# Kernel tuning notes

Measured on AMD Instinct MI355X. Metric: run time of the kernel, lower is better.

Reference implementation:

```python
import jax, jax.numpy as jnp
import numpy as np
import math

B, H, S, D = 2, 16, 2048, 64

def setup_inputs() -> dict:
    key = jax.random.key(0)
    kq, kk, kv = jax.random.split(key, 3)
    Q = jax.random.normal(kq, (B, H, S, D), dtype=jnp.float32)
    K = jax.random.normal(kk, (B, H, S, D), dtype=jnp.float32)
    V = jax.random.normal(kv, (B, H, S, D), dtype=jnp.float32)
    causal_mask = jnp.tril(jnp.ones((S, S), dtype=bool))
    return {"Q": Q, "K": K, "V": V, "causal_mask": causal_mask}

def reference(Q, K, V, causal_mask):
    d_k = K.shape[-1]
    scores = jnp.einsum('bhqd,bhkd->bhqk', Q, K) / math.sqrt(d_k)
    scores = jnp.where(causal_mask, scores, -jnp.inf)
    probs = jax.nn.softmax(scores, axis=-1)
    return jnp.einsum('bhqk,bhkd->bhqd', probs, V)
```

## Files before the change

kernel.cpp:

```cpp
#include <hip/hip_runtime.h>
#include <math.h>


constexpr int kS   = 2048;
constexpr int kD   = 64;
constexpr int kBH  = 32;
constexpr int kPadP = 72;
constexpr int kFragBH = 64 * 4 * 512;

typedef short short8 __attribute__((ext_vector_type(8)));
typedef float float4v __attribute__((ext_vector_type(4)));
typedef float float16v __attribute__((ext_vector_type(16)));
typedef unsigned int u32;
typedef unsigned short u16;

static __device__ inline u16 f2bf(float f) {
  union { float f; unsigned u; } v; v.f = f;
  unsigned r = v.u + 0x7FFF + ((v.u >> 16) & 1);
  return (u16)(r >> 16);
}

static __device__ inline short8 pack8(float4v a, float4v b) {
  short8 r;
  r[0] = (short)f2bf(a[0]); r[1] = (short)f2bf(a[1]);
  r[2] = (short)f2bf(a[2]); r[3] = (short)f2bf(a[3]);
  r[4] = (short)f2bf(b[0]); r[5] = (short)f2bf(b[1]);
  r[6] = (short)f2bf(b[2]); r[7] = (short)f2bf(b[3]);
  return r;
}

static __device__ inline void swap32(u32 a, u32 b, u32& oa, u32& ob) {
#if __has_builtin(__builtin_amdgcn_permlane32_swap)
  auto r = __builtin_amdgcn_permlane32_swap(a, b, false, false);
  oa = r[0]; ob = r[1];
#else
  asm volatile("v_permlane32_swap_b32 %0, %1" : "+v"(a), "+v"(b));
  oa = a; ob = b;
#endif
}

__global__ __launch_bounds__(256)
void prep_kernel(const float* __restrict__ Q, const float* __restrict__ K,
                 const float* __restrict__ V,
                 u16* __restrict__ Qf, u16* __restrict__ Kf, u16* __restrict__ Vf) {
  __shared__ u16 tile[64 * kPadP];
  const int tid = threadIdx.x;
  const int bh = blockIdx.y, st = blockIdx.x;
  const size_t ibase = (size_t)bh * kS * kD + (size_t)st * 64 * kD;
  const size_t fbase = (size_t)bh * kFragBH;
  const int r  = tid >> 2;
  const int c0 = (tid & 3) * 16;
  const int dk = tid & 3;
  const int U  = st * 2 + (r >> 5);
  const int lr = r & 31;
  {
    const float scl = 0.125f * 1.44269504089f;
    const float* qp = Q + ibase + (size_t)r * kD + c0;
    float4v a = *(const float4v*)(qp);
    float4v b = *(const float4v*)(qp + 4);
    float4v c = *(const float4v*)(qp + 8);
    float4v d = *(const float4v*)(qp + 12);
    #pragma unroll
    for (int i = 0; i < 4; ++i) { a[i] *= scl; b[i] *= scl; c[i] *= scl; d[i] *= scl; }
    u16* dst = Qf + fbase + (size_t)(U * 4 + dk) * 512;
    *(short8*)(dst + lr * 8)        = pack8(a, b);
    *(short8*)(dst + (32 + lr) * 8) = pack8(c, d);
  }
  {
    const float* kp = K + ibase + (size_t)r * kD + c0;
    float4v a = *(const float4v*)(kp);
    float4v b = *(const float4v*)(kp + 4);
    float4v c = *(const float4v*)(kp + 8);
    float4v d = *(const float4v*)(kp + 12);
    u16* dst = Kf + fbase + (size_t)(U * 4 + dk) * 512;
    *(short8*)(dst + lr * 8)        = pack8(a, b);
    *(short8*)(dst + (32 + lr) * 8) = pack8(c, d);
  }
  {
    const float* vp = V + ibase + (size_t)r * kD + c0;
    float4v a = *(const float4v*)(vp);
    float4v b = *(const float4v*)(vp + 4);
    float4v c = *(const float4v*)(vp + 8);
    float4v d = *(const float4v*)(vp + 12);
    u16* t = &tile[r * kPadP + c0];
    *(short8*)t       = pack8(a, b);
    *(short8*)(t + 8) = pack8(c, d);
  }
  __syncthreads();
  {
    const int dd = tid >> 2;
    const int s0 = (tid & 3) * 16;
    short8 w0, w1;
    #pragma unroll
    for (int i = 0; i < 8; ++i) {
      w0[i] = (short)tile[(s0 + i) * kPadP + dd];
      w1[i] = (short)tile[(s0 + 8 + i) * kPadP + dd];
    }
    const int ku   = st * 2 + (s0 >> 5);
    const int koff = s0 & 31;
    const int c    = ((koff >> 4) << 1) | (dd >> 5);
    u16* vdst = Vf + fbase + (size_t)(ku * 4 + c) * 512;
    *(short8*)(vdst + (dd & 31) * 8)        = w0;
    *(short8*)(vdst + (32 + (dd & 31)) * 8) = w1;
  }
}

__global__ __launch_bounds__(64, 2)
void fattn_kernel(const u16* __restrict__ Qf, const u16* __restrict__ Kf,
                  const u16* __restrict__ Vf, float* __restrict__ O) {
  const int lane = threadIdx.x;
  const int l31  = lane & 31;
  const int h    = lane >> 5;

  const int orig = ((blockIdx.x & 7) << 8) | (blockIdx.x >> 3);
  const int pr   = orig >> 7;
  const int r2   = orig & 127;
  const int s    = 63 - (r2 >> 1);
  const int bh   = pr * 2 + (r2 & 1);
  const int q0   = s * 32;

  const size_t fb = (size_t)bh * kFragBH;
  const u16* kp = Kf + fb + lane * 8;
  const u16* vp = Vf + fb + lane * 8;

  float16v zf;
  #pragma unroll
  for (int i = 0; i < 16; ++i) zf[i] = 0.f;

  short8 ones;
  #pragma unroll
  for (int i = 0; i < 8; ++i) ones[i] = (short)0x3F80;

  short8 qf[4];
  {
    const u16* qp = Qf + fb + (size_t)(s * 4) * 512 + lane * 8;
    #pragma unroll
    for (int dk = 0; dk < 4; ++dk) qf[dk] = *(const short8*)(qp + dk * 512);
  }

  float16v acc0 = zf, acc1 = zf, lacc = zf;
  const int qg = q0 + l31;

  short8 kA[4], vA[4], kB[4], vB[4];
  #pragma unroll
  for (int dk = 0; dk < 4; ++dk) kA[dk] = *(const short8*)(kp + dk * 512);
  #pragma unroll
  for (int c = 0; c < 4; ++c)    vA[c]  = *(const short8*)(vp + c * 512);

  auto step = [&](const short8* kc, const short8* vc, short8* kn, short8* vn, int k) {
    const int knext = (k < s) ? (k + 1) : k;
    #pragma unroll
    for (int dk = 0; dk < 4; ++dk) kn[dk] = *(const short8*)(kp + knext * 2048 + dk * 512);
    #pragma unroll
    for (int c = 0; c < 4; ++c)    vn[c]  = *(const short8*)(vp + knext * 2048 + c * 512);

    __builtin_amdgcn_s_setprio(1);
    float16v sv = __builtin_amdgcn_mfma_f32_32x32x16_bf16(kc[0], qf[0], zf, 0, 0, 0);
    sv = __builtin_amdgcn_mfma_f32_32x32x16_bf16(kc[1], qf[1], sv, 0, 0, 0);
    sv = __builtin_amdgcn_mfma_f32_32x32x16_bf16(kc[2], qf[2], sv, 0, 0, 0);
    sv = __builtin_amdgcn_mfma_f32_32x32x16_bf16(kc[3], qf[3], sv, 0, 0, 0);
    __builtin_amdgcn_s_setprio(0);

    if (k == s) {
      #pragma unroll
      for (int r = 0; r < 16; ++r) {
        const int kg = k * 32 + (r & 3) + 8 * (r >> 2) + 4 * h;
        if (kg > qg) sv[r] = -1e30f;
      }
    }

    u32 pk[8];
    #pragma unroll
    for (int g2 = 0; g2 < 4; ++g2) {
      const u32 u0 = __float_as_uint(__builtin_amdgcn_exp2f(sv[4 * g2 + 0]));
      const u32 u1 = __float_as_uint(__builtin_amdgcn_exp2f(sv[4 * g2 + 1]));
      const u32 u2 = __float_as_uint(__builtin_amdgcn_exp2f(sv[4 * g2 + 2]));
      const u32 u3 = __float_as_uint(__builtin_amdgcn_exp2f(sv[4 * g2 + 3]));
      pk[2 * g2]     = __builtin_amdgcn_perm(u1, u0, 0x07060302u);
      pk[2 * g2 + 1] = __builtin_amdgcn_perm(u3, u2, 0x07060302u);
    }

    {
      union { u32 u[4]; short8 s8; } pf;
      swap32(pk[0], pk[2], pf.u[0], pf.u[2]);
      swap32(pk[1], pk[3], pf.u[1], pf.u[3]);
      __builtin_amdgcn_s_setprio(1);
      acc0 = __builtin_amdgcn_mfma_f32_32x32x16_bf16(pf.s8, vc[0], acc0, 0, 0, 0);
      acc1 = __builtin_amdgcn_mfma_f32_32x32x16_bf16(pf.s8, vc[1], acc1, 0, 0, 0);
      lacc = __builtin_amdgcn_mfma_f32_32x32x16_bf16(pf.s8, ones,  lacc, 0, 0, 0);
      __builtin_amdgcn_s_setprio(0);
    }
    {
      union { u32 u[4]; short8 s8; } pf;
      swap32(pk[4], pk[6], pf.u[0], pf.u[2]);
      swap32(pk[5], pk[7], pf.u[1], pf.u[3]);
      __builtin_amdgcn_s_setprio(1);
      acc0 = __builtin_amdgcn_mfma_f32_32x32x16_bf16(pf.s8, vc[2], acc0, 0, 0, 0);
      acc1 = __builtin_amdgcn_mfma_f32_32x32x16_bf16(pf.s8, vc[3], acc1, 0, 0, 0);
      lacc = __builtin_amdgcn_mfma_f32_32x32x16_bf16(pf.s8, ones,  lacc, 0, 0, 0);
      __builtin_amdgcn_s_setprio(0);
    }
  };

  int k = 0;
  while (true) {
    step(kA, vA, kB, vB, k); if (++k > s) break;
    step(kB, vB, kA, vA, k); if (++k > s) break;
  }

  #pragma unroll
  for (int r = 0; r < 16; ++r) {
    const int row = (r & 3) + 8 * (r >> 2) + 4 * h;
    const float inv = 1.f / lacc[r];
    float* op = O + ((size_t)bh * kS + q0 + row) * kD;
    op[l31]      = acc0[r] * inv;
    op[l31 + 32] = acc1[r] * inv;
  }
}

extern "C" void kernel_launch(void* const* d_in, const int* in_sizes, int n_in,
                              void* d_out, int out_size, void* d_ws, size_t ws_size,
                              hipStream_t stream) {
  const float* Q = (const float*)d_in[0];
  const float* K = (const float*)d_in[1];
  const float* V = (const float*)d_in[2];
  float* O = (float*)d_out;

  const size_t nKV = (size_t)kBH * kS * kD;
  u16* Qf = (u16*)d_ws;
  u16* Kf = Qf + nKV;
  u16* Vf = Kf + nKV;

  dim3 gprep(kS / 64, kBH);
  prep_kernel<<<gprep, 256, 0, stream>>>(Q, K, V, Qf, Kf, Vf);
  fattn_kernel<<<2048, 64, 0, stream>>>(Qf, Kf, Vf, O);
}
```

Measured before the change: 142.9 us.

## Pair short and long causal query tiles per wave to share K/V loads

Each wave now processes two query tiles, sA and the mirrored 63-sA, so every wave does the same amount of causal work and reuses each K/V fragment load for both tiles while k<=sA. The launch moves from 2048 single-wave blocks to 256 four-wave blocks. K/V prefetch uses inline-asm global_load_dwordx4 with explicit vmcnt waits and sched barriers. This removes load imbalance across the causal triangle and cuts global K/V traffic. The cost is fewer, fatter waves with doubled accumulator registers (only 256 blocks for the GPU) and more fragile hand-managed waits.

```diff
diff --git a/kernel.cpp b/kernel.cpp
--- a/kernel.cpp
+++ b/kernel.cpp
@@ -12,6 +12,7 @@
 typedef float float4v __attribute__((ext_vector_type(4)));
 typedef float float16v __attribute__((ext_vector_type(16)));
 typedef unsigned int u32;
+typedef unsigned int u32x4 __attribute__((ext_vector_type(4)));
 typedef unsigned short u16;
 
 static __device__ inline u16 f2bf(float f) {
@@ -37,6 +38,13 @@
   asm volatile("v_permlane32_swap_b32 %0, %1" : "+v"(a), "+v"(b));
   oa = a; ob = b;
 #endif
+}
+
+static __device__ inline void gload16(u32x4& d, const u16* p) {
+  asm volatile("global_load_dwordx4 %0, %1, off" : "=v"(d) : "v"(p));
+}
+static __device__ inline short8 asfrag(u32x4 u) {
+  union { u32x4 u; short8 s; } c; c.u = u; return c.s;
 }
 
 __global__ __launch_bounds__(256)
@@ -105,23 +113,27 @@
   }
 }
 
-__global__ __launch_bounds__(64, 2)
+__global__ __launch_bounds__(256, 1)
 void fattn_kernel(const u16* __restrict__ Qf, const u16* __restrict__ Kf,
                   const u16* __restrict__ Vf, float* __restrict__ O) {
-  const int lane = threadIdx.x;
+  const int tid  = threadIdx.x;
+  const int wave = tid >> 6;
+  const int lane = tid & 63;
   const int l31  = lane & 31;
   const int h    = lane >> 5;
 
-  const int orig = ((blockIdx.x & 7) << 8) | (blockIdx.x >> 3);
-  const int pr   = orig >> 7;
-  const int r2   = orig & 127;
-  const int s    = 63 - (r2 >> 1);
-  const int bh   = pr * 2 + (r2 & 1);
-  const int q0   = s * 32;
+  const int b   = blockIdx.x;
+  const int m   = b >> 3;
+  const int bh  = (b & 7) * 4 + (m & 3);
+  const int sg  = m >> 2;
+  const int sA  = sg * 4 + wave;
+  const int sB  = 63 - sA;
+  const int q0A = sA * 32, q0B = sB * 32;
+  const int kend = sB;
 
   const size_t fb = (size_t)bh * kFragBH;
-  const u16* kp = Kf + fb + lane * 8;
-  const u16* vp = Vf + fb + lane * 8;
+  const u16* gk = Kf + fb + lane * 8;
+  const u16* gv = Vf + fb + lane * 8;
 
   float16v zf;
   #pragma unroll
@@ -131,37 +143,40 @@
   #pragma unroll
   for (int i = 0; i < 8; ++i) ones[i] = (short)0x3F80;
 
-  short8 qf[4];
-  {
-    const u16* qp = Qf + fb + (size_t)(s * 4) * 512 + lane * 8;
-    #pragma unroll
-    for (int dk = 0; dk < 4; ++dk) qf[dk] = *(const short8*)(qp + dk * 512);
-  }
-
-  float16v acc0 = zf, acc1 = zf, lacc = zf;
-  const int qg = q0 + l31;
-
-  short8 kA[4], vA[4], kB[4], vB[4];
-  #pragma unroll
-  for (int dk = 0; dk < 4; ++dk) kA[dk] = *(const short8*)(kp + dk * 512);
-  #pragma unroll
-  for (int c = 0; c < 4; ++c)    vA[c]  = *(const short8*)(vp + c * 512);
-
-  auto step = [&](const short8* kc, const short8* vc, short8* kn, short8* vn, int k) {
-    const int knext = (k < s) ? (k + 1) : k;
-    #pragma unroll
-    for (int dk = 0; dk < 4; ++dk) kn[dk] = *(const short8*)(kp + knext * 2048 + dk * 512);
-    #pragma unroll
-    for (int c = 0; c < 4; ++c)    vn[c]  = *(const short8*)(vp + knext * 2048 + c * 512);
-
+  short8 qfA[4], qfB[4];
+  {
+    const u16* qa = Qf + fb + (size_t)(sA * 4) * 512 + lane * 8;
+    const u16* qb = Qf + fb + (size_t)(sB * 4) * 512 + lane * 8;
+    #pragma unroll
+    for (int dk = 0; dk < 4; ++dk) {
+      qfA[dk] = *(const short8*)(qa + dk * 512);
+      qfB[dk] = *(const short8*)(qb + dk * 512);
+    }
+  }
+
+  float16v a0A = zf, a1A = zf, laA = zf;
+  float16v a0B = zf, a1B = zf, laB = zf;
+  const int qgA = q0A + l31, qgB = q0B + l31;
+
+  u32x4 kX[4], vX[4], kY[4], vY[4];
+
+  #pragma unroll
+  for (int i = 0; i < 4; ++i) gload16(kX[i], gk + i * 512);
+  #pragma unroll
+  for (int i = 0; i < 4; ++i) gload16(vX[i], gv + i * 512);
+  asm volatile("s_waitcnt vmcnt(0)" ::: "memory");
+  __builtin_amdgcn_sched_barrier(0);
+
+  auto doSet = [&](const short8* qf, float16v& a0, float16v& a1, float16v& la,
+                   int qg, int sdiag, int k, const u32x4* kc, const u32x4* vc) {
     __builtin_amdgcn_s_setprio(1);
-    float16v sv = __builtin_amdgcn_mfma_f32_32x32x16_bf16(kc[0], qf[0], zf, 0, 0, 0);
-    sv = __builtin_amdgcn_mfma_f32_32x32x16_bf16(kc[1], qf[1], sv, 0, 0, 0);
-    sv = __builtin_amdgcn_mfma_f32_32x32x16_bf16(kc[2], qf[2], sv, 0, 0, 0);
-    sv = __builtin_amdgcn_mfma_f32_32x32x16_bf16(kc[3], qf[3], sv, 0, 0, 0);
+    float16v sv = __builtin_amdgcn_mfma_f32_32x32x16_bf16(asfrag(kc[0]), qf[0], zf, 0, 0, 0);
+    sv = __builtin_amdgcn_mfma_f32_32x32x16_bf16(asfrag(kc[1]), qf[1], sv, 0, 0, 0);
+    sv = __builtin_amdgcn_mfma_f32_32x32x16_bf16(asfrag(kc[2]), qf[2], sv, 0, 0, 0);
+    sv = __builtin_amdgcn_mfma_f32_32x32x16_bf16(asfrag(kc[3]), qf[3], sv, 0, 0, 0);
     __builtin_amdgcn_s_setprio(0);
 
-    if (k == s) {
+    if (k == sdiag) {
       #pragma unroll
       for (int r = 0; r < 16; ++r) {
         const int kg = k * 32 + (r & 3) + 8 * (r >> 2) + 4 * h;
@@ -185,9 +200,9 @@
       swap32(pk[0], pk[2], pf.u[0], pf.u[2]);
       swap32(pk[1], pk[3], pf.u[1], pf.u[3]);
       __builtin_amdgcn_s_setprio(1);
-      acc0 = __builtin_amdgcn_mfma_f32_32x32x16_bf16(pf.s8, vc[0], acc0, 0, 0, 0);
-      acc1 = __builtin_amdgcn_mfma_f32_32x32x16_bf16(pf.s8, vc[1], acc1, 0, 0, 0);
-      lacc = __builtin_amdgcn_mfma_f32_32x32x16_bf16(pf.s8, ones,  lacc, 0, 0, 0);
+      a0 = __builtin_amdgcn_mfma_f32_32x32x16_bf16(pf.s8, asfrag(vc[0]), a0, 0, 0, 0);
+      a1 = __builtin_amdgcn_mfma_f32_32x32x16_bf16(pf.s8, asfrag(vc[1]), a1, 0, 0, 0);
+      la = __builtin_amdgcn_mfma_f32_32x32x16_bf16(pf.s8, ones,          la, 0, 0, 0);
       __builtin_amdgcn_s_setprio(0);
     }
     {
@@ -195,26 +210,51 @@
       swap32(pk[4], pk[6], pf.u[0], pf.u[2]);
       swap32(pk[5], pk[7], pf.u[1], pf.u[3]);
       __builtin_amdgcn_s_setprio(1);
-      acc0 = __builtin_amdgcn_mfma_f32_32x32x16_bf16(pf.s8, vc[2], acc0, 0, 0, 0);
-      acc1 = __builtin_amdgcn_mfma_f32_32x32x16_bf16(pf.s8, vc[3], acc1, 0, 0, 0);
-      lacc = __builtin_amdgcn_mfma_f32_32x32x16_bf16(pf.s8, ones,  lacc, 0, 0, 0);
+      a0 = __builtin_amdgcn_mfma_f32_32x32x16_bf16(pf.s8, asfrag(vc[2]), a0, 0, 0, 0);
+      a1 = __builtin_amdgcn_mfma_f32_32x32x16_bf16(pf.s8, asfrag(vc[3]), a1, 0, 0, 0);
+      la = __builtin_amdgcn_mfma_f32_32x32x16_bf16(pf.s8, ones,          la, 0, 0, 0);
       __builtin_amdgcn_s_setprio(0);
     }
   };
 
+  auto unit = [&](const u32x4* kc, const u32x4* vc, u32x4* kn, u32x4* vn, int k) {
+    if (k < kend) {
+      const u16* pk_ = gk + (size_t)(k + 1) * 2048;
+      const u16* pv_ = gv + (size_t)(k + 1) * 2048;
+      #pragma unroll
+      for (int i = 0; i < 4; ++i) gload16(kn[i], pk_ + i * 512);
+      #pragma unroll
+      for (int i = 0; i < 4; ++i) gload16(vn[i], pv_ + i * 512);
+      asm volatile("s_waitcnt vmcnt(8)" ::: "memory");
+    } else {
+      asm volatile("s_waitcnt vmcnt(0)" ::: "memory");
+    }
+    __builtin_amdgcn_sched_barrier(0);
+
+    doSet(qfB, a0B, a1B, laB, qgB, sB, k, kc, vc);
+    if (k <= sA)
+      doSet(qfA, a0A, a1A, laA, qgA, sA, k, kc, vc);
+  };
+
   int k = 0;
-  while (true) {
-    step(kA, vA, kB, vB, k); if (++k > s) break;
-    step(kB, vB, kA, vA, k); if (++k > s) break;
+  for (;;) {
+    unit(kX, vX, kY, vY, k);
+    if (++k > kend) break;
+    unit(kY, vY, kX, vX, k);
+    if (++k > kend) break;
   }
 
   #pragma unroll
   for (int r = 0; r < 16; ++r) {
     const int row = (r & 3) + 8 * (r >> 2) + 4 * h;
-    const float inv = 1.f / lacc[r];
-    float* op = O + ((size_t)bh * kS + q0 + row) * kD;
-    op[l31]      = acc0[r] * inv;
-    op[l31 + 32] = acc1[r] * inv;
+    const float invA = 1.f / laA[r];
+    const float invB = 1.f / laB[r];
+    float* opA = O + ((size_t)bh * kS + q0A + row) * kD;
+    float* opB = O + ((size_t)bh * kS + q0B + row) * kD;
+    opA[l31]      = a0A[r] * invA;
+    opA[l31 + 32] = a1A[r] * invA;
+    opB[l31]      = a0B[r] * invB;
+    opB[l31 + 32] = a1B[r] * invB;
   }
 }
 
@@ -233,5 +273,5 @@
 
   dim3 gprep(kS / 64, kBH);
   prep_kernel<<<gprep, 256, 0, stream>>>(Q, K, V, Qf, Kf, Vf);
-  fattn_kernel<<<2048, 64, 0, stream>>>(Qf, Kf, Vf, O);
-}
+  fattn_kernel<<<256, 256, 0, stream>>>(Qf, Kf, Vf, O);
+}
```

Result: slower. 155.5 us (+8.8%).

## Pair causal query tiles per block and split key work evenly across waves

Applied to the files above, without the earlier changes.

Each 256-thread block now handles two query tiles, s and 63-s, whose causal work together is a constant 65 key blocks. The block's four waves each take a contiguous quarter of that combined range. Partial numerators (stored as bf16) and row sums go to shared memory, then the block merges them and normalizes before writing the output. This is meant to remove the load imbalance between short and long causal rows. It also replaces the row-sum MFMA with VALU adds and drops the register double-buffered K/V prefetch, so it relies on higher occupancy to hide memory latency, and storing partials in bf16 adds rounding error.

```diff
diff --git a/kernel.cpp b/kernel.cpp
--- a/kernel.cpp
+++ b/kernel.cpp
@@ -105,63 +105,85 @@
   }
 }
 
-__global__ __launch_bounds__(64, 2)
+__global__ __launch_bounds__(256, 3)
 void fattn_kernel(const u16* __restrict__ Qf, const u16* __restrict__ Kf,
                   const u16* __restrict__ Vf, float* __restrict__ O) {
-  const int lane = threadIdx.x;
+  __shared__ u32   ldsP[5][32][33];
+  __shared__ float ldsL[5][32];
+
+  const int tid  = threadIdx.x;
+  const int wave = tid >> 6;
+  const int lane = tid & 63;
   const int l31  = lane & 31;
   const int h    = lane >> 5;
 
-  const int orig = ((blockIdx.x & 7) << 8) | (blockIdx.x >> 3);
-  const int pr   = orig >> 7;
-  const int r2   = orig & 127;
-  const int s    = 63 - (r2 >> 1);
-  const int bh   = pr * 2 + (r2 & 1);
-  const int q0   = s * 32;
+  const int blk = blockIdx.x;
+  const int bh  = (blk & 7) * 4 + ((blk >> 3) & 3);
+  const int sA  = blk >> 5;
+  const int sB  = 63 - sA;
+  const int t   = sB + 1;
+  const int lo  = (65 * wave) >> 2;
+  const int hi  = (65 * (wave + 1)) >> 2;
 
   const size_t fb = (size_t)bh * kFragBH;
-  const u16* kp = Kf + fb + lane * 8;
-  const u16* vp = Vf + fb + lane * 8;
+  const u16* gk = Kf + fb + lane * 8;
+  const u16* gv = Vf + fb + lane * 8;
 
   float16v zf;
   #pragma unroll
   for (int i = 0; i < 16; ++i) zf[i] = 0.f;
 
-  short8 ones;
-  #pragma unroll
-  for (int i = 0; i < 8; ++i) ones[i] = (short)0x3F80;
+  int scur = (lo < t) ? sB : sA;
+  int koff = (lo < t) ? 0 : t;
 
   short8 qf[4];
   {
-    const u16* qp = Qf + fb + (size_t)(s * 4) * 512 + lane * 8;
+    const u16* qp = Qf + fb + (size_t)(scur * 4) * 512 + lane * 8;
     #pragma unroll
     for (int dk = 0; dk < 4; ++dk) qf[dk] = *(const short8*)(qp + dk * 512);
   }
 
-  float16v acc0 = zf, acc1 = zf, lacc = zf;
-  const int qg = q0 + l31;
-
-  short8 kA[4], vA[4], kB[4], vB[4];
-  #pragma unroll
-  for (int dk = 0; dk < 4; ++dk) kA[dk] = *(const short8*)(kp + dk * 512);
-  #pragma unroll
-  for (int c = 0; c < 4; ++c)    vA[c]  = *(const short8*)(vp + c * 512);
-
-  auto step = [&](const short8* kc, const short8* vc, short8* kn, short8* vn, int k) {
-    const int knext = (k < s) ? (k + 1) : k;
-    #pragma unroll
-    for (int dk = 0; dk < 4; ++dk) kn[dk] = *(const short8*)(kp + knext * 2048 + dk * 512);
-    #pragma unroll
-    for (int c = 0; c < 4; ++c)    vn[c]  = *(const short8*)(vp + knext * 2048 + c * 512);
+  float16v acc0 = zf, acc1 = zf;
+  float lac = 0.f;
+
+  auto dump = [&](int slot) {
+    #pragma unroll
+    for (int r = 0; r < 16; ++r) {
+      const int row = (r & 3) + 8 * (r >> 2) + 4 * h;
+      ldsP[slot][row][l31] = (u32)f2bf(acc0[r]) | ((u32)f2bf(acc1[r]) << 16);
+    }
+    const float lt = lac + __shfl_xor(lac, 32);
+    if (lane < 32) ldsL[slot][lane] = lt;
+  };
+
+  for (int u = lo; u < hi; ++u) {
+    if (u == t && u != lo) {
+      dump(wave);
+      acc0 = zf; acc1 = zf; lac = 0.f;
+      scur = sA; koff = t;
+      const u16* qp = Qf + fb + (size_t)(sA * 4) * 512 + lane * 8;
+      #pragma unroll
+      for (int dk = 0; dk < 4; ++dk) qf[dk] = *(const short8*)(qp + dk * 512);
+    }
+    const int k = u - koff;
+
+    const u16* kp = gk + (size_t)k * 2048;
+    const u16* vp = gv + (size_t)k * 2048;
+    short8 kf[4], vf[4];
+    #pragma unroll
+    for (int i = 0; i < 4; ++i) kf[i] = *(const short8*)(kp + i * 512);
+    #pragma unroll
+    for (int i = 0; i < 4; ++i) vf[i] = *(const short8*)(vp + i * 512);
 
     __builtin_amdgcn_s_setprio(1);
-    float16v sv = __builtin_amdgcn_mfma_f32_32x32x16_bf16(kc[0], qf[0], zf, 0, 0, 0);
-    sv = __builtin_amdgcn_mfma_f32_32x32x16_bf16(kc[1], qf[1], sv, 0, 0, 0);
-    sv = __builtin_amdgcn_mfma_f32_32x32x16_bf16(kc[2], qf[2], sv, 0, 0, 0);
-    sv = __builtin_amdgcn_mfma_f32_32x32x16_bf16(kc[3], qf[3], sv, 0, 0, 0);
+    float16v sv = __builtin_amdgcn_mfma_f32_32x32x16_bf16(kf[0], qf[0], zf, 0, 0, 0);
+    sv = __builtin_amdgcn_mfma_f32_32x32x16_bf16(kf[1], qf[1], sv, 0, 0, 0);
+    sv = __builtin_amdgcn_mfma_f32_32x32x16_bf16(kf[2], qf[2], sv, 0, 0, 0);
+    sv = __builtin_amdgcn_mfma_f32_32x32x16_bf16(kf[3], qf[3], sv, 0, 0, 0);
     __builtin_amdgcn_s_setprio(0);
 
-    if (k == s) {
+    if (k == scur) {
+      const int qg = scur * 32 + l31;
       #pragma unroll
       for (int r = 0; r < 16; ++r) {
         const int kg = k * 32 + (r & 3) + 8 * (r >> 2) + 4 * h;
@@ -181,13 +203,23 @@
     }
 
     {
+      float e[8];
+      #pragma unroll
+      for (int i = 0; i < 8; ++i)
+        e[i] = __uint_as_float(pk[i] << 16)
+             + __uint_as_float(pk[i] & 0xFFFF0000u);
+      e[0] += e[1]; e[2] += e[3]; e[4] += e[5]; e[6] += e[7];
+      e[0] += e[2]; e[4] += e[6];
+      lac += e[0] + e[4];
+    }
+
+    {
       union { u32 u[4]; short8 s8; } pf;
       swap32(pk[0], pk[2], pf.u[0], pf.u[2]);
       swap32(pk[1], pk[3], pf.u[1], pf.u[3]);
       __builtin_amdgcn_s_setprio(1);
-      acc0 = __builtin_amdgcn_mfma_f32_32x32x16_bf16(pf.s8, vc[0], acc0, 0, 0, 0);
-      acc1 = __builtin_amdgcn_mfma_f32_32x32x16_bf16(pf.s8, vc[1], acc1, 0, 0, 0);
-      lacc = __builtin_amdgcn_mfma_f32_32x32x16_bf16(pf.s8, ones,  lacc, 0, 0, 0);
+      acc0 = __builtin_amdgcn_mfma_f32_32x32x16_bf16(pf.s8, vf[0], acc0, 0, 0, 0);
+      acc1 = __builtin_amdgcn_mfma_f32_32x32x16_bf16(pf.s8, vf[1], acc1, 0, 0, 0);
       __builtin_amdgcn_s_setprio(0);
     }
     {
@@ -195,26 +227,49 @@
       swap32(pk[4], pk[6], pf.u[0], pf.u[2]);
       swap32(pk[5], pk[7], pf.u[1], pf.u[3]);
       __builtin_amdgcn_s_setprio(1);
-      acc0 = __builtin_amdgcn_mfma_f32_32x32x16_bf16(pf.s8, vc[2], acc0, 0, 0, 0);
-      acc1 = __builtin_amdgcn_mfma_f32_32x32x16_bf16(pf.s8, vc[3], acc1, 0, 0, 0);
-      lacc = __builtin_amdgcn_mfma_f32_32x32x16_bf16(pf.s8, ones,  lacc, 0, 0, 0);
+      acc0 = __builtin_amdgcn_mfma_f32_32x32x16_bf16(pf.s8, vf[2], acc0, 0, 0, 0);
+      acc1 = __builtin_amdgcn_mfma_f32_32x32x16_bf16(pf.s8, vf[3], acc1, 0, 0, 0);
       __builtin_amdgcn_s_setprio(0);
     }
-  };
-
-  int k = 0;
-  while (true) {
-    step(kA, vA, kB, vB, k); if (++k > s) break;
-    step(kB, vB, kA, vA, k); if (++k > s) break;
-  }
-
-  #pragma unroll
-  for (int r = 0; r < 16; ++r) {
-    const int row = (r & 3) + 8 * (r >> 2) + 4 * h;
-    const float inv = 1.f / lacc[r];
-    float* op = O + ((size_t)bh * kS + q0 + row) * kD;
-    op[l31]      = acc0[r] * inv;
-    op[l31 + 32] = acc1[r] * inv;
+  }
+
+  dump((lo < t && t < hi) ? 4 : wave);
+
+  __syncthreads();
+
+  {
+    const int setid = tid >> 7;
+    const int sOut  = setid ? sA : sB;
+    const bool v0 = setid ? (0  >= t) : (0  < t);
+    const bool v1 = setid ? (16 >= t) : (16 < t);
+    const bool v2 = setid ? (32 >= t) : (32 < t);
+    const bool v3 = setid ? (48 >= t) : (48 < t);
+    const bool v4 = (setid != 0) && (t != 48);
+
+    const int q  = (tid & 127) >> 2;
+    const int c0 = (tid & 3) * 8;
+
+    float lsum = 0.f;
+    if (v0) lsum += ldsL[0][q];
+    if (v1) lsum += ldsL[1][q];
+    if (v2) lsum += ldsL[2][q];
+    if (v3) lsum += ldsL[3][q];
+    if (v4) lsum += ldsL[4][q];
+    const float inv = 1.f / lsum;
+
+    float* op = O + ((size_t)bh * kS + sOut * 32 + q) * kD;
+    #pragma unroll
+    for (int i = 0; i < 8; ++i) {
+      const int c = c0 + i;
+      float lov = 0.f, hiv = 0.f;
+      if (v0) { const u32 p = ldsP[0][q][c]; lov += __uint_as_float(p << 16); hiv += __uint_as_float(p & 0xFFFF0000u); }
+      if (v1) { const u32 p = ldsP[1][q][c]; lov += __uint_as_float(p << 16); hiv += __uint_as_float(p & 0xFFFF0000u); }
+      if (v2) { const u32 p = ldsP[2][q][c]; lov += __uint_as_float(p << 16); hiv += __uint_as_float(p & 0xFFFF0000u); }
+      if (v3) { const u32 p = ldsP[3][q][c]; lov += __uint_as_float(p << 16); hiv += __uint_as_float(p & 0xFFFF0000u); }
+      if (v4) { const u32 p = ldsP[4][q][c]; lov += __uint_as_float(p << 16); hiv += __uint_as_float(p & 0xFFFF0000u); }
+      op[c]      = lov * inv;
+      op[c + 32] = hiv * inv;
+    }
   }
 }
 
@@ -233,5 +288,5 @@
 
   dim3 gprep(kS / 64, kBH);
   prep_kernel<<<gprep, 256, 0, stream>>>(Q, K, V, Qf, Kf, Vf);
-  fattn_kernel<<<2048, 64, 0, stream>>>(Qf, Kf, Vf, O);
-}
+  fattn_kernel<<<1024, 256, 0, stream>>>(Qf, Kf, Vf, O);
+}
```

Result: faster. 136.0 us (-4.8%).
